# Optimization experiments

Measured on AMD Instinct MI355X. Metric: run time of the kernel, lower is better.

## Reference

```python
import jax, jax.numpy as jnp
import numpy as np

B = 256      # graph pairs
N = 256      # nodes per graph (uniform -> padding is a reshape)
DEG = 16     # avg degree
D = 32       # one_hot_dim
F1, F2, F3 = 128, 64, 64
T = 16       # tensor_neurons
BINS = 16
BOT = 16     # bottle_neck_neurons


def setup_inputs() -> dict:
    key = jax.random.key(0)
    ks = jax.random.split(key, 24)
    NT = B * N            # total nodes per side
    NE = B * N * DEG      # total directed edges per side
    x_q = jax.random.normal(ks[0], (NT, D), jnp.float32)
    x_c = jax.random.normal(ks[1], (NT, D), jnp.float32)
    edge_q = jax.random.randint(ks[2], (2, NE), 0, NT, jnp.int32)
    edge_c = jax.random.randint(ks[3], (2, NE), 0, NT, jnp.int32)
    qgraph_sizes = jnp.full((B,), N, jnp.int32)
    cgraph_sizes = jnp.full((B,), N, jnp.int32)

    def glorot(k, shape):
        fan = sum(shape[-2:]) if len(shape) >= 2 else shape[0] * 2
        return jax.random.uniform(k, shape, jnp.float32, -1.0, 1.0) * np.sqrt(6.0 / fan)

    params = dict(
        W1=glorot(ks[4], (D, F1)), b1=jnp.zeros((F1,), jnp.float32),
        W2=glorot(ks[5], (F1, F2)), b2=jnp.zeros((F2,), jnp.float32),
        W3=glorot(ks[6], (F2, F3)), b3=jnp.zeros((F3,), jnp.float32),
        attn_w=glorot(ks[7], (F3, F3)),
        ntn_a_w=glorot(ks[8], (T, F3, F3)),
        ntn_b_w=glorot(ks[9], (2 * F3, T)),
        ntn_bias=glorot(ks[10], (T, 1)),
        fc1_w=glorot(ks[11], (T + BINS, BOT)), fc1_b=jnp.zeros((BOT,), jnp.float32),
        fc2_w=glorot(ks[12], (BOT, 1)), fc2_b=jnp.zeros((1,), jnp.float32),
    )
    return dict(x_q=x_q, edge_q=edge_q, x_c=x_c, edge_c=edge_c,
                qgraph_sizes=qgraph_sizes, cgraph_sizes=cgraph_sizes, **params)


def _gcn(x, src, dst, W, b):
    n = x.shape[0]
    h = x @ W
    loop = jnp.arange(n, dtype=src.dtype)
    s = jnp.concatenate([src, loop])
    d = jnp.concatenate([dst, loop])
    deg = jax.ops.segment_sum(jnp.ones(s.shape, h.dtype), d, num_segments=n)
    dinv = jnp.where(deg > 0, jax.lax.rsqrt(jnp.maximum(deg, 1.0)), 0.0)
    coef = (dinv[s] * dinv[d])[:, None]
    return jax.ops.segment_sum(h[s] * coef, d, num_segments=n) + b


def _gnn(x, ei, W1, b1, W2, b2, W3, b3):
    src, dst = ei[0], ei[1]
    h = jax.nn.relu(_gcn(x, src, dst, W1, b1))        # dropout is identity in eval
    h = jax.nn.relu(_gcn(h, src, dst, W2, b2))
    return _gcn(h, src, dst, W3, b3)                  # [B*N, F3]


def _att_pool(q, attn_w, sizes):
    # q: [B, N, F3]
    ctx = jnp.tanh((q.sum(axis=1) @ attn_w) / sizes.astype(q.dtype)[:, None])  # [B, F3]
    sig = jax.nn.sigmoid(jnp.einsum('bnf,bf->bn', q, ctx))                      # [B, N]
    return jnp.einsum('bnf,bn->bf', q, sig)                                     # [B, F3]


def _pair_hist(q, c):
    # per-pair histogram of q @ c^T with BINS bins over each pair's [min, max]
    s = jax.lax.stop_gradient(jnp.einsum('bnf,bmf->bnm', q, c))  # [B, N, N]
    mn = s.min(axis=(1, 2), keepdims=True)
    mx = s.max(axis=(1, 2), keepdims=True)
    idx = jnp.clip(jnp.floor((s - mn) / jnp.maximum(mx - mn, 1e-12) * BINS),
                   0, BINS - 1).astype(jnp.int32)
    gid = (idx + jnp.arange(B, dtype=jnp.int32)[:, None, None] * BINS).reshape(-1)
    h = jax.ops.segment_sum(jnp.ones(gid.shape, jnp.float32), gid,
                            num_segments=B * BINS).reshape(B, BINS)
    return h / h.sum(axis=1, keepdims=True)


def reference(x_q, edge_q, x_c, edge_c, qgraph_sizes, cgraph_sizes,
              W1, b1, W2, b2, W3, b3, attn_w, ntn_a_w, ntn_b_w, ntn_bias,
              fc1_w, fc1_b, fc2_w, fc2_b):
    q = _gnn(x_q, edge_q, W1, b1, W2, b2, W3, b3).reshape(B, N, F3)
    c = _gnn(x_c, edge_c, W1, b1, W2, b2, W3, b3).reshape(B, N, F3)
    e1 = _att_pool(q, attn_w, qgraph_sizes)
    e2 = _att_pool(c, attn_w, cgraph_sizes)
    ntn = (jnp.einsum('bi,tij,bj->bt', e1, ntn_a_w, e2)
           + jnp.concatenate([e1, e2], axis=-1) @ ntn_b_w
           + ntn_bias[:, 0])
    scores = jax.nn.relu(ntn)                                   # [B, T]
    hist = _pair_hist(q, c)                                     # [B, BINS]
    scores = jnp.concatenate([scores, hist], axis=1)
    scores = jax.nn.relu(scores @ fc1_w + fc1_b)
    p = jax.nn.sigmoid(scores @ fc2_w + fc2_b)[:, 0]            # [B]
    ged = -0.5 * (qgraph_sizes + cgraph_sizes).astype(p.dtype) * jnp.log(p)
    return ged
```

## Files before the change

kernel.cpp:

```cpp
#include <hip/hip_runtime.h>
#include <hip/hip_bf16.h>
#include <math.h>

#define BB 256
#define NN 256
#define NT (BB*NN)
#define NT2 (2*NT)
#define NE (NT*16)
#define DD 32
#define F1C 128
#define F2C 64
#define F3C 64
#define TT 16
#define BINS 16

#define NBUCK 256
#define BSHIFT 9
#define BNODES 512
#define BCAP 10240
#define EPB 4096

typedef __attribute__((ext_vector_type(8))) short short8;
typedef __attribute__((ext_vector_type(4))) float f32x4;
typedef __attribute__((ext_vector_type(2))) float f32x2;

__device__ inline float b2f(ushort u) { return __uint_as_float(((uint)u) << 16); }
__device__ inline ushort f2b(float f) {
    uint u = __float_as_uint(f);
    return (ushort)((u + 0x7fffu + ((u >> 16) & 1u)) >> 16);
}
__device__ inline float clamp8(float v) { return fminf(fmaxf(v, -448.0f), 448.0f); }
__device__ inline uchar f2f8(float v) {
    int r = __builtin_amdgcn_cvt_pk_fp8_f32(clamp8(v), 0.0f, 0, false);
    return (uchar)(r & 0xff);
}
__device__ inline void f8x8_acc(uint2 w, float* acc) {
    f32x2 p;
    p = __builtin_amdgcn_cvt_pk_f32_fp8(w.x, false); acc[0] += p.x; acc[1] += p.y;
    p = __builtin_amdgcn_cvt_pk_f32_fp8(w.x, true);  acc[2] += p.x; acc[3] += p.y;
    p = __builtin_amdgcn_cvt_pk_f32_fp8(w.y, false); acc[4] += p.x; acc[5] += p.y;
    p = __builtin_amdgcn_cvt_pk_f32_fp8(w.y, true);  acc[6] += p.x; acc[7] += p.y;
}
__device__ inline uint2 f8x8_pack(const float* v) {
    uint2 r;
    r.x = (uint)__builtin_amdgcn_cvt_pk_fp8_f32(clamp8(v[0]), clamp8(v[1]), 0, false);
    r.x = (uint)__builtin_amdgcn_cvt_pk_fp8_f32(clamp8(v[2]), clamp8(v[3]), (int)r.x, true);
    r.y = (uint)__builtin_amdgcn_cvt_pk_fp8_f32(clamp8(v[4]), clamp8(v[5]), 0, false);
    r.y = (uint)__builtin_amdgcn_cvt_pk_fp8_f32(clamp8(v[6]), clamp8(v[7]), (int)r.y, true);
    return r;
}

__global__ __launch_bounds__(256) void prep_k(const float* __restrict__ W1, const float* __restrict__ W2,
                                              const float* __restrict__ W3, ushort* __restrict__ Wt1,
                                              ushort* __restrict__ Wt2, uchar* __restrict__ Wt3f8,
                                              int* __restrict__ gcount) {
    int i = blockIdx.x * 256 + threadIdx.x;
    if (i < NBUCK) gcount[i] = 0;
    if (i < DD * F1C)  { int k = i / F1C, n = i % F1C; Wt1[n * DD + k]  = f2b(W1[i]); }
    if (i < F1C * F2C) { int k = i / F2C, n = i % F2C; Wt2[n * F1C + k] = f2b(W2[i]); }
    if (i < F2C * F3C) { int k = i / F3C, n = i % F3C; Wt3f8[n * F2C + k] = f2f8(W3[i]); }
}

__global__ __launch_bounds__(256) void csr_p1_k(const int* __restrict__ eq, const int* __restrict__ ec,
                                                uint* __restrict__ staged, int* __restrict__ gcount) {
    __shared__ uint s_pk[EPB];
    __shared__ int s_cnt[NBUCK];
    __shared__ int s_off[NBUCK];
    __shared__ int s_base[NBUCK];
    __shared__ int s_gb[NBUCK];
    int t = threadIdx.x;
    bool sideB = blockIdx.x >= 256;
    const int* edge = sideB ? ec : eq;
    int off = sideB ? NT : 0;
    int e0 = (blockIdx.x & 255) * EPB;
    s_cnt[t] = 0;
    __syncthreads();
    uint pk[16]; int bk[16];
#pragma unroll
    for (int j = 0; j < 16; j++) {
        int e = e0 + j * 256 + t;
        int s = edge[e] + off;
        int d = edge[NE + e] + off;
        bk[j] = d >> BSHIFT;
        pk[j] = ((uint)s << BSHIFT) | (uint)(d & (BNODES - 1));
        atomicAdd(&s_cnt[bk[j]], 1);
    }
    __syncthreads();
    s_off[t] = s_cnt[t];
    __syncthreads();
    for (int o = 1; o < NBUCK; o <<= 1) {
        int x = (t >= o) ? s_off[t - o] : 0;
        __syncthreads();
        s_off[t] += x;
        __syncthreads();
    }
    {
        int ex = s_off[t] - s_cnt[t];
        s_base[t] = ex;
        s_off[t] = ex;
        s_gb[t] = atomicAdd(&gcount[t], s_cnt[t]);
    }
    __syncthreads();
#pragma unroll
    for (int j = 0; j < 16; j++) {
        int pos = atomicAdd(&s_off[bk[j]], 1);
        s_pk[pos] = pk[j];
    }
    __syncthreads();
    int w = t >> 6, l = t & 63;
    int bsel = l >> 4, l16 = l & 15;
    for (int pb = w; pb < NBUCK / 4; pb += 4) {
        int b = pb * 4 + bsel;
        int n = s_cnt[b], st = s_base[b], gb = s_gb[b];
        if (gb + n > BCAP) n = max(0, BCAP - gb);
        for (int i = l16; i < n; i += 16)
            staged[b * BCAP + gb + i] = s_pk[st + i];
    }
}

__global__ __launch_bounds__(256) void csr_p2_k(const uint* __restrict__ staged, const int* __restrict__ gcount,
                                                int* __restrict__ rp, int* __restrict__ indeg,
                                                float* __restrict__ dinv, int* __restrict__ ep) {
    int b = blockIdx.x;
    int t = threadIdx.x;
    __shared__ int cnt[BNODES];
    __shared__ int fl[BNODES];
    __shared__ int wsum[256];
    __shared__ int gsc[NBUCK];
    cnt[t] = 0; cnt[t + 256] = 0;
    gsc[t] = min(gcount[t], BCAP);
    __syncthreads();
    for (int off = 1; off < NBUCK; off <<= 1) {
        int x = (t >= off) ? gsc[t - off] : 0;
        __syncthreads();
        gsc[t] += x;
        __syncthreads();
    }
    int gbase = (b == 0) ? 0 : gsc[b - 1];
    int n = min(gcount[b], BCAP);
    const uint* sb = staged + (size_t)b * BCAP;
    int i = t;
    for (; i + 768 < n; i += 1024) {
        uint p0 = sb[i];
        uint p1 = sb[i + 256];
        uint p2 = sb[i + 512];
        uint p3 = sb[i + 768];
        atomicAdd(&cnt[p0 & (BNODES - 1)], 1);
        atomicAdd(&cnt[p1 & (BNODES - 1)], 1);
        atomicAdd(&cnt[p2 & (BNODES - 1)], 1);
        atomicAdd(&cnt[p3 & (BNODES - 1)], 1);
    }
    for (; i < n; i += 256)
        atomicAdd(&cnt[sb[i] & (BNODES - 1)], 1);
    __syncthreads();
    int base2 = t * 2;
    int c0 = cnt[base2], c1 = cnt[base2 + 1];
    int s2 = c0 + c1;
    wsum[t] = s2;
    __syncthreads();
    for (int off = 1; off < 256; off <<= 1) {
        int x = (t >= off) ? wsum[t - off] : 0;
        __syncthreads();
        wsum[t] += x;
        __syncthreads();
    }
    int p = gbase + wsum[t] - s2;
    int v0 = b * BNODES + base2;
    rp[v0] = p;          fl[base2] = p;
    indeg[v0] = c0;      dinv[v0] = rsqrtf((float)(c0 + 1));
    p += c0;
    rp[v0 + 1] = p;      fl[base2 + 1] = p;
    indeg[v0 + 1] = c1;  dinv[v0 + 1] = rsqrtf((float)(c1 + 1));
    __syncthreads();
    i = t;
    for (; i + 768 < n; i += 1024) {
        uint p0 = sb[i];
        uint p1 = sb[i + 256];
        uint p2 = sb[i + 512];
        uint p3 = sb[i + 768];
        ep[atomicAdd(&fl[p0 & (BNODES - 1)], 1)] = (int)(p0 >> BSHIFT);
        ep[atomicAdd(&fl[p1 & (BNODES - 1)], 1)] = (int)(p1 >> BSHIFT);
        ep[atomicAdd(&fl[p2 & (BNODES - 1)], 1)] = (int)(p2 >> BSHIFT);
        ep[atomicAdd(&fl[p3 & (BNODES - 1)], 1)] = (int)(p3 >> BSHIFT);
    }
    for (; i < n; i += 256) {
        uint pk = sb[i];
        ep[atomicAdd(&fl[pk & (BNODES - 1)], 1)] = (int)(pk >> BSHIFT);
    }
}

__global__ __launch_bounds__(256) void cvt2_k(const float* __restrict__ a, const float* __restrict__ b,
                                              const float* __restrict__ dinv, ushort* __restrict__ out) {
    int i = blockIdx.x * 256 + threadIdx.x;
    const int per = NT * DD / 4;
    bool sideB = i >= per;
    const float4* src = (const float4*)(sideB ? b : a);
    float4 v = src[sideB ? i - per : i];
    float dv = dinv[i / (DD / 4)];
    ushort4 o;
    o.x = f2b(v.x * dv); o.y = f2b(v.y * dv); o.z = f2b(v.z * dv); o.w = f2b(v.w * dv);
    ((ushort4*)out)[i] = o;
}

template<int F, bool BIAS, bool RELU>
__global__ __launch_bounds__(256) void agg_bf_k(const ushort* __restrict__ in, const int* __restrict__ rp,
                                                const int* __restrict__ indeg, const int* __restrict__ ep,
                                                const float* __restrict__ dinv,
                                                const float* __restrict__ bias, ushort* __restrict__ out) {
    constexpr int LPV = F / 8;
    constexpr int VPB = 256 / LPV;
    int g = threadIdx.x / LPV;
    int l = threadIdx.x % LPV;
    int v = blockIdx.x * VPB + g;
    float dv = dinv[v];
    short8 rs = *(const short8*)(in + (size_t)v * F + l * 8);
    float acc[8];
#pragma unroll
    for (int j = 0; j < 8; j++) acc[j] = b2f((ushort)rs[j]);
    int start = rp[v];
    int cnt   = indeg[v];
    int i = 0;
    for (; i + 4 <= cnt; i += 4) {
        int s0 = ep[start + i];
        int s1 = ep[start + i + 1];
        int s2 = ep[start + i + 2];
        int s3 = ep[start + i + 3];
        short8 r0 = *(const short8*)(in + (size_t)s0 * F + l * 8);
        short8 r1 = *(const short8*)(in + (size_t)s1 * F + l * 8);
        short8 r2 = *(const short8*)(in + (size_t)s2 * F + l * 8);
        short8 r3 = *(const short8*)(in + (size_t)s3 * F + l * 8);
#pragma unroll
        for (int j = 0; j < 8; j++) {
            acc[j] += b2f((ushort)r0[j]);
            acc[j] += b2f((ushort)r1[j]);
            acc[j] += b2f((ushort)r2[j]);
            acc[j] += b2f((ushort)r3[j]);
        }
    }
    for (; i < cnt; i++) {
        int s0 = ep[start + i];
        short8 r0 = *(const short8*)(in + (size_t)s0 * F + l * 8);
#pragma unroll
        for (int j = 0; j < 8; j++) acc[j] += b2f((ushort)r0[j]);
    }
    short8 o;
#pragma unroll
    for (int j = 0; j < 8; j++) {
        float x = dv * acc[j];
        if (BIAS) x += bias[l * 8 + j];
        if (RELU) x = fmaxf(x, 0.0f);
        o[j] = (short)f2b(x);
    }
    *(short8*)(out + (size_t)v * F + l * 8) = o;
}

template<bool OUT_BF16, bool BIAS, bool RELU>
__global__ __launch_bounds__(256) void agg_f8_k(const uchar* __restrict__ in, const int* __restrict__ rp,
                                                const int* __restrict__ indeg, const int* __restrict__ ep,
                                                const float* __restrict__ dinv,
                                                const float* __restrict__ bias, void* __restrict__ outp) {
    int g = threadIdx.x >> 3;
    int l = threadIdx.x & 7;
    int v = blockIdx.x * 32 + g;
    float dv = dinv[v];
    float acc[8] = {0, 0, 0, 0, 0, 0, 0, 0};
    f8x8_acc(*(const uint2*)(in + (size_t)v * 64 + l * 8), acc);
    int start = rp[v];
    int cnt   = indeg[v];
    int i = 0;
    for (; i + 4 <= cnt; i += 4) {
        int s0 = ep[start + i];
        int s1 = ep[start + i + 1];
        int s2 = ep[start + i + 2];
        int s3 = ep[start + i + 3];
        uint2 g0 = *(const uint2*)(in + (size_t)s0 * 64 + l * 8);
        uint2 g1 = *(const uint2*)(in + (size_t)s1 * 64 + l * 8);
        uint2 g2 = *(const uint2*)(in + (size_t)s2 * 64 + l * 8);
        uint2 g3 = *(const uint2*)(in + (size_t)s3 * 64 + l * 8);
        f8x8_acc(g0, acc); f8x8_acc(g1, acc); f8x8_acc(g2, acc); f8x8_acc(g3, acc);
    }
    for (; i < cnt; i++) {
        int s0 = ep[start + i];
        f8x8_acc(*(const uint2*)(in + (size_t)s0 * 64 + l * 8), acc);
    }
#pragma unroll
    for (int j = 0; j < 8; j++) {
        float x = dv * acc[j];
        if (BIAS) x += bias[l * 8 + j];
        if (RELU) x = fmaxf(x, 0.0f);
        acc[j] = x;
    }
    if (OUT_BF16) {
        short8 o;
#pragma unroll
        for (int j = 0; j < 8; j++) o[j] = (short)f2b(acc[j]);
        *(short8*)((ushort*)outp + (size_t)v * 64 + l * 8) = o;
    } else {
        *(uint2*)((uchar*)outp + (size_t)v * 64 + l * 8) = f8x8_pack(acc);
    }
}

template<int K, int N, bool BIAS, bool RELU, bool SCALE, bool OUT8>
__global__ __launch_bounds__(256) void gemm_mfma_k(const ushort* __restrict__ A,
                                                   const ushort* __restrict__ Wt,
                                                   const float* __restrict__ bias,
                                                   const float* __restrict__ dinv,
                                                   void* __restrict__ outp) {
    constexpr int KC = K / 32;
    int w = threadIdx.x >> 6, lane = threadIdx.x & 63;
    int r16 = lane & 15, koff = (lane >> 4) * 8;
    size_t rows0 = (size_t)blockIdx.x * 128;

    short8 af[KC][2];
#pragma unroll
    for (int kc = 0; kc < KC; kc++)
#pragma unroll
        for (int mt = 0; mt < 2; mt++)
            af[kc][mt] = *(const short8*)(A + (rows0 + (w * 2 + mt) * 16 + r16) * K + kc * 32 + koff);

    float dvr[2][4];
#pragma unroll
    for (int mt = 0; mt < 2; mt++)
#pragma unroll
        for (int r = 0; r < 4; r++)
            dvr[mt][r] = SCALE ? dinv[rows0 + (w * 2 + mt) * 16 + (lane >> 4) * 4 + r] : 1.0f;

#pragma unroll
    for (int nt = 0; nt < N / 16; nt++) {
        f32x4 acc[2] = {{0.f,0.f,0.f,0.f},{0.f,0.f,0.f,0.f}};
#pragma unroll
        for (int kc = 0; kc < KC; kc++) {
            short8 b = *(const short8*)(Wt + (size_t)(nt * 16 + r16) * K + kc * 32 + koff);
            acc[0] = __builtin_amdgcn_mfma_f32_16x16x32_bf16(af[kc][0], b, acc[0], 0, 0, 0);
            acc[1] = __builtin_amdgcn_mfma_f32_16x16x32_bf16(af[kc][1], b, acc[1], 0, 0, 0);
        }
#pragma unroll
        for (int mt = 0; mt < 2; mt++) {
#pragma unroll
            for (int r = 0; r < 4; r++) {
                size_t row = rows0 + (w * 2 + mt) * 16 + (lane >> 4) * 4 + r;
                int col = nt * 16 + (lane & 15);
                float v = acc[mt][r];
                if (BIAS) v += bias[col];
                if (RELU) v = fmaxf(v, 0.0f);
                if (SCALE) v *= dvr[mt][r];
                if (OUT8) ((uchar*)outp)[row * N + col] = f2f8(v);
                else      ((ushort*)outp)[row * N + col] = f2b(v);
            }
        }
    }
}

__global__ __launch_bounds__(256) void gemm_f8_k(const uchar* __restrict__ A8,
                                                 const uchar* __restrict__ Wt8,
                                                 const float* __restrict__ dinv,
                                                 uchar* __restrict__ out8) {
    int w = threadIdx.x >> 6, lane = threadIdx.x & 63;
    int r16 = lane & 15, koff = (lane >> 4) * 8;
    size_t rows0 = (size_t)blockIdx.x * 128;

    long af[2][2];
#pragma unroll
    for (int kc = 0; kc < 2; kc++)
#pragma unroll
        for (int mt = 0; mt < 2; mt++)
            af[kc][mt] = *(const long*)(A8 + (rows0 + (w * 2 + mt) * 16 + r16) * 64 + kc * 32 + koff);

    float dvr[2][4];
#pragma unroll
    for (int mt = 0; mt < 2; mt++)
#pragma unroll
        for (int r = 0; r < 4; r++)
            dvr[mt][r] = dinv[rows0 + (w * 2 + mt) * 16 + (lane >> 4) * 4 + r];

#pragma unroll
    for (int nt = 0; nt < 4; nt++) {
        f32x4 acc[2] = {{0.f,0.f,0.f,0.f},{0.f,0.f,0.f,0.f}};
#pragma unroll
        for (int kc = 0; kc < 2; kc++) {
            long b = *(const long*)(Wt8 + (size_t)(nt * 16 + r16) * 64 + kc * 32 + koff);
            acc[0] = __builtin_amdgcn_mfma_f32_16x16x32_fp8_fp8(af[kc][0], b, acc[0], 0, 0, 0);
            acc[1] = __builtin_amdgcn_mfma_f32_16x16x32_fp8_fp8(af[kc][1], b, acc[1], 0, 0, 0);
        }
#pragma unroll
        for (int mt = 0; mt < 2; mt++) {
#pragma unroll
            for (int r = 0; r < 4; r++) {
                size_t row = rows0 + (w * 2 + mt) * 16 + (lane >> 4) * 4 + r;
                int col = nt * 16 + (lane & 15);
                out8[row * 64 + col] = f2f8(acc[mt][r] * dvr[mt][r]);
            }
        }
    }
}

__global__ __launch_bounds__(256) void pool_k(const ushort* __restrict__ fin,
                                              const int* __restrict__ qsz, const int* __restrict__ csz,
                                              const float* __restrict__ attn_w, float* __restrict__ e_out) {
    int b = blockIdx.x & 255;
    bool is_c = blockIdx.x >= BB;
    const ushort* emb = fin + (size_t)blockIdx.x * NN * F3C;
    float size = (float)((is_c ? csz : qsz)[b]);
    float* eo = e_out + (is_c ? BB * F3C : 0) + b * F3C;

    int t = threadIdx.x;
    int f = t & 63;
    int w = t >> 6;

    __shared__ float s_emb[NN][F3C + 1];
    __shared__ float s_red[4][64];
    __shared__ float s_sq[64];
    __shared__ float s_ctx[64];
    __shared__ float s_sig[NN];

    float psum = 0.0f;
    for (int n = w; n < NN; n += 4) {
        float v = b2f(emb[n * F3C + f]);
        s_emb[n][f] = v;
        psum += v;
    }
    s_red[w][f] = psum;
    __syncthreads();

    if (w == 0) {
        s_sq[f] = s_red[0][f] + s_red[1][f] + s_red[2][f] + s_red[3][f];
        float acc = 0.0f;
        for (int k = 0; k < 64; k++) acc += s_sq[k] * attn_w[k * 64 + f];
        s_ctx[f] = tanhf(acc / size);
    }
    __syncthreads();

    {
        float acc = 0.0f;
#pragma unroll 8
        for (int k = 0; k < 64; k++) acc += s_emb[t][k] * s_ctx[k];
        s_sig[t] = 1.0f / (1.0f + expf(-acc));
    }
    __syncthreads();

    float eacc = 0.0f;
#pragma unroll 8
    for (int i = 0; i < 64; i++) {
        int n = w * 64 + i;
        eacc += s_sig[n] * s_emb[n][f];
    }
    s_red[w][f] = eacc;
    __syncthreads();
    if (w == 0) eo[f] = s_red[0][f] + s_red[1][f] + s_red[2][f] + s_red[3][f];
}

__global__ __launch_bounds__(256) void hist_k(const ushort* __restrict__ qbf, const ushort* __restrict__ cbf,
                                              float* __restrict__ histp) {
    int b = blockIdx.x;
    const ushort* qb = qbf + (size_t)b * NN * 64;
    const ushort* cb = cbf + (size_t)b * NN * 64;
    int lane = threadIdx.x & 63;
    int w = threadIdx.x >> 6;
    int r16 = lane & 15, koff = (lane >> 4) * 8;

    short8 a[4][2];
#pragma unroll
    for (int i = 0; i < 4; i++) {
        int row = (w * 4 + i) * 16 + r16;
#pragma unroll
        for (int kk = 0; kk < 2; kk++)
            a[i][kk] = *(const short8*)(qb + row * 64 + kk * 32 + koff);
    }

    float mn = 1e30f, mx = -1e30f;
    for (int mt = 0; mt < 16; mt++) {
        int crow = mt * 16 + r16;
        short8 b0 = *(const short8*)(cb + crow * 64 + koff);
        short8 b1 = *(const short8*)(cb + crow * 64 + 32 + koff);
#pragma unroll
        for (int i = 0; i < 4; i++) {
            f32x4 acc = {0.0f, 0.0f, 0.0f, 0.0f};
            acc = __builtin_amdgcn_mfma_f32_16x16x32_bf16(a[i][0], b0, acc, 0, 0, 0);
            acc = __builtin_amdgcn_mfma_f32_16x16x32_bf16(a[i][1], b1, acc, 0, 0, 0);
            mn = fminf(mn, fminf(fminf(acc[0], acc[1]), fminf(acc[2], acc[3])));
            mx = fmaxf(mx, fmaxf(fmaxf(acc[0], acc[1]), fmaxf(acc[2], acc[3])));
        }
    }
    for (int off = 32; off; off >>= 1) {
        mn = fminf(mn, __shfl_xor(mn, off, 64));
        mx = fmaxf(mx, __shfl_xor(mx, off, 64));
    }
    __shared__ float smn[4], smx[4];
    __shared__ float s_mn, s_scale;
    if (lane == 0) { smn[w] = mn; smx[w] = mx; }
    __syncthreads();
    if (threadIdx.x == 0) {
        float m0 = fminf(fminf(smn[0], smn[1]), fminf(smn[2], smn[3]));
        float m1 = fmaxf(fmaxf(smx[0], smx[1]), fmaxf(smx[2], smx[3]));
        s_mn = m0;
        s_scale = 16.0f / fmaxf(m1 - m0, 1e-12f);
    }
    __shared__ int h[16 * 256];
#pragma unroll
    for (int i = 0; i < 16; i++) h[i * 256 + threadIdx.x] = 0;
    __syncthreads();
    float bmn = s_mn, bscale = s_scale;

    for (int mt = 0; mt < 16; mt++) {
        int crow = mt * 16 + r16;
        short8 b0 = *(const short8*)(cb + crow * 64 + koff);
        short8 b1 = *(const short8*)(cb + crow * 64 + 32 + koff);
#pragma unroll
        for (int i = 0; i < 4; i++) {
            f32x4 acc = {0.0f, 0.0f, 0.0f, 0.0f};
            acc = __builtin_amdgcn_mfma_f32_16x16x32_bf16(a[i][0], b0, acc, 0, 0, 0);
            acc = __builtin_amdgcn_mfma_f32_16x16x32_bf16(a[i][1], b1, acc, 0, 0, 0);
#pragma unroll
            for (int r = 0; r < 4; r++) {
                int bin = (int)floorf((acc[r] - bmn) * bscale);
                bin = min(max(bin, 0), 15);
                h[bin * 256 + threadIdx.x] += 1;
            }
        }
    }
    __syncthreads();
    __shared__ int hp[16][16];
    int bb = threadIdx.x >> 4, part = threadIdx.x & 15;
    int sum = 0;
#pragma unroll
    for (int j = 0; j < 16; j++) sum += h[bb * 256 + part * 16 + j];
    hp[bb][part] = sum;
    __syncthreads();
    if (threadIdx.x < 16) {
        int s = 0;
#pragma unroll
        for (int j = 0; j < 16; j++) s += hp[threadIdx.x][j];
        histp[b * 16 + threadIdx.x] = (float)s;
    }
}

__global__ __launch_bounds__(256) void ntn_final_k(const float* __restrict__ e, const float* __restrict__ A,
                                                   const float* __restrict__ bw, const float* __restrict__ bias,
                                                   const float* __restrict__ histp,
                                                   const float* __restrict__ fc1w, const float* __restrict__ fc1b,
                                                   const float* __restrict__ fc2w, const float* __restrict__ fc2b,
                                                   const int* __restrict__ qsz, const int* __restrict__ csz,
                                                   float* __restrict__ out) {
    int b = blockIdx.x;
    int t = threadIdx.x;
    __shared__ float s_e1[64], s_e2[64];
    __shared__ float s_ntn[16];
    __shared__ float s_s[32];
    __shared__ float s_a[16];
    if (t < 64) s_e1[t] = e[b * 64 + t];
    else if (t < 128) s_e2[t - 64] = e[BB * 64 + b * 64 + (t - 64)];
    if (t < 16) s_ntn[t] = 0.0f;
    __syncthreads();
#pragma unroll
    for (int r = 0; r < 4; r++) {
        int idx = t + r * 256;
        int tt = idx >> 6, i = idx & 63;
        const float* Ar = A + (size_t)idx * 64;
        float acc = 0.0f;
        for (int j = 0; j < 64; j++) acc += Ar[j] * s_e2[j];
        atomicAdd(&s_ntn[tt], s_e1[i] * acc);
    }
    __syncthreads();
    if (t < 16) {
        float acc = s_ntn[t] + bias[t];
        for (int k = 0; k < 64; k++) acc += s_e1[k] * bw[k * 16 + t];
        for (int k = 0; k < 64; k++) acc += s_e2[k] * bw[(64 + k) * 16 + t];
        s_s[t] = fmaxf(acc, 0.0f);
        s_s[16 + t] = histp[b * 16 + t] * (1.0f / 65536.0f);
    }
    __syncthreads();
    if (t < 16) {
        float a = fc1b[t];
        for (int k = 0; k < 32; k++) a += s_s[k] * fc1w[k * 16 + t];
        s_a[t] = fmaxf(a, 0.0f);
    }
    __syncthreads();
    if (t == 0) {
        float z = fc2b[0];
        for (int j = 0; j < 16; j++) z += s_a[j] * fc2w[j];
        float nz = -z;
        float sp = (nz > 20.0f) ? nz : log1pf(expf(nz));
        out[b] = 0.5f * (float)(qsz[b] + csz[b]) * sp;
    }
}

extern "C" void kernel_launch(void* const* d_in, const int* in_sizes, int n_in,
                              void* d_out, int out_size, void* d_ws, size_t ws_size,
                              hipStream_t stream) {
    const float* x_q    = (const float*)d_in[0];
    const int*   edge_q = (const int*)d_in[1];
    const float* x_c    = (const float*)d_in[2];
    const int*   edge_c = (const int*)d_in[3];
    const int*   qsz    = (const int*)d_in[4];
    const int*   csz    = (const int*)d_in[5];
    const float* W1 = (const float*)d_in[6];
    const float* b1 = (const float*)d_in[7];
    const float* W2 = (const float*)d_in[8];
    const float* b2 = (const float*)d_in[9];
    const float* W3 = (const float*)d_in[10];
    const float* b3 = (const float*)d_in[11];
    const float* attn_w  = (const float*)d_in[12];
    const float* ntn_a   = (const float*)d_in[13];
    const float* ntn_b   = (const float*)d_in[14];
    const float* ntn_bias= (const float*)d_in[15];
    const float* fc1w = (const float*)d_in[16];
    const float* fc1b = (const float*)d_in[17];
    const float* fc2w = (const float*)d_in[18];
    const float* fc2b = (const float*)d_in[19];
    float* out = (float*)d_out;

    char* w = (char*)d_ws;
    auto alloc = [&](size_t bytes) -> void* {
        void* p = (void*)w;
        w += (bytes + 255) & ~(size_t)255;
        return p;
    };
    int*    rp     = (int*)alloc((size_t)NT2 * 4);
    int*    indeg  = (int*)alloc((size_t)NT2 * 4);
    float*  dinv   = (float*)alloc((size_t)NT2 * 4);
    int*    gcount = (int*)alloc(NBUCK * 4);
    uint*   staged = (uint*)alloc((size_t)NBUCK * BCAP * 4);
    int*    ep     = (int*)alloc((size_t)2 * NE * 4);
    ushort* xb     = (ushort*)alloc((size_t)NT2 * 32 * 2);
    ushort* xa     = (ushort*)alloc((size_t)NT2 * 32 * 2);
    ushort* hA     = (ushort*)alloc((size_t)NT2 * 128 * 2);
    uchar*  h8a    = (uchar*)alloc((size_t)NT2 * 64);
    uchar*  h8b    = (uchar*)alloc((size_t)NT2 * 64);
    ushort* fin    = (ushort*)alloc((size_t)NT2 * 64 * 2);
    ushort* Wt1    = (ushort*)alloc((size_t)DD * F1C * 2);
    ushort* Wt2    = (ushort*)alloc((size_t)F1C * F2C * 2);
    uchar*  Wt3f8  = (uchar*)alloc((size_t)F2C * F3C);
    float*  e12    = (float*)alloc(2 * BB * 64 * 4);
    float*  histp  = (float*)alloc(256 * 16 * 4);
    ushort* qfin = fin;
    ushort* cfin = fin + (size_t)NT * 64;

    prep_k<<<32, 256, 0, stream>>>(W1, W2, W3, Wt1, Wt2, Wt3f8, gcount);
    csr_p1_k<<<512, 256, 0, stream>>>(edge_q, edge_c, staged, gcount);
    csr_p2_k<<<NBUCK, 256, 0, stream>>>(staged, gcount, rp, indeg, dinv, ep);

    cvt2_k<<<NT2 * 32 / 4 / 256, 256, 0, stream>>>(x_q, x_c, dinv, xb);

    agg_bf_k<32, false, false><<<NT2 / 64, 256, 0, stream>>>(xb, rp, indeg, ep, dinv, nullptr, xa);
    gemm_mfma_k<32, 128, true, true, false, false><<<NT2 / 128, 256, 0, stream>>>(xa, Wt1, b1, nullptr, hA);
    gemm_mfma_k<128, 64, false, false, true, true><<<NT2 / 128, 256, 0, stream>>>(hA, Wt2, nullptr, dinv, h8a);
    agg_f8_k<false, true, true><<<NT2 / 32, 256, 0, stream>>>(h8a, rp, indeg, ep, dinv, b2, h8b);
    gemm_f8_k<<<NT2 / 128, 256, 0, stream>>>(h8b, Wt3f8, dinv, h8a);
    agg_f8_k<true, true, false><<<NT2 / 32, 256, 0, stream>>>(h8a, rp, indeg, ep, dinv, b3, fin);

    pool_k<<<2 * BB, 256, 0, stream>>>(fin, qsz, csz, attn_w, e12);
    hist_k<<<BB, 256, 0, stream>>>(qfin, cfin, histp);
    ntn_final_k<<<BB, 256, 0, stream>>>(e12, ntn_a, ntn_b, ntn_bias, histp,
                                        fc1w, fc1b, fc2w, fc2b, qsz, csz, out);
}
```

Measured before the change: 319.4 us.

## Fuse layer-1/2 GEMMs through LDS and merge small kernels

```diff
diff --git a/kernel.cpp b/kernel.cpp
--- a/kernel.cpp
+++ b/kernel.cpp
@@ -50,15 +50,8 @@
     return r;
 }
 
-__global__ __launch_bounds__(256) void prep_k(const float* __restrict__ W1, const float* __restrict__ W2,
-                                              const float* __restrict__ W3, ushort* __restrict__ Wt1,
-                                              ushort* __restrict__ Wt2, uchar* __restrict__ Wt3f8,
-                                              int* __restrict__ gcount) {
-    int i = blockIdx.x * 256 + threadIdx.x;
-    if (i < NBUCK) gcount[i] = 0;
-    if (i < DD * F1C)  { int k = i / F1C, n = i % F1C; Wt1[n * DD + k]  = f2b(W1[i]); }
-    if (i < F1C * F2C) { int k = i / F2C, n = i % F2C; Wt2[n * F1C + k] = f2b(W2[i]); }
-    if (i < F2C * F3C) { int k = i / F3C, n = i % F3C; Wt3f8[n * F2C + k] = f2f8(W3[i]); }
+__global__ __launch_bounds__(256) void zero_k(int* __restrict__ gcount) {
+    gcount[threadIdx.x] = 0;
 }
 
 __global__ __launch_bounds__(256) void csr_p1_k(const int* __restrict__ eq, const int* __restrict__ ec,
@@ -189,17 +182,28 @@
     }
 }
 
-__global__ __launch_bounds__(256) void cvt2_k(const float* __restrict__ a, const float* __restrict__ b,
-                                              const float* __restrict__ dinv, ushort* __restrict__ out) {
-    int i = blockIdx.x * 256 + threadIdx.x;
-    const int per = NT * DD / 4;
-    bool sideB = i >= per;
-    const float4* src = (const float4*)(sideB ? b : a);
-    float4 v = src[sideB ? i - per : i];
-    float dv = dinv[i / (DD / 4)];
-    ushort4 o;
-    o.x = f2b(v.x * dv); o.y = f2b(v.y * dv); o.z = f2b(v.z * dv); o.w = f2b(v.w * dv);
-    ((ushort4*)out)[i] = o;
+__global__ __launch_bounds__(256) void cvt2w_k(const float* __restrict__ a, const float* __restrict__ b,
+                                               const float* __restrict__ dinv, ushort* __restrict__ out,
+                                               const float* __restrict__ W1, const float* __restrict__ W2,
+                                               const float* __restrict__ W3, ushort* __restrict__ Wt1,
+                                               ushort* __restrict__ Wt2, uchar* __restrict__ Wt3f8) {
+    const int NB_X = NT2 * DD / 4 / 256;
+    if (blockIdx.x < NB_X) {
+        int i = blockIdx.x * 256 + threadIdx.x;
+        const int per = NT * DD / 4;
+        bool sideB = i >= per;
+        const float4* src = (const float4*)(sideB ? b : a);
+        float4 v = src[sideB ? i - per : i];
+        float dv = dinv[i / (DD / 4)];
+        ushort4 o;
+        o.x = f2b(v.x * dv); o.y = f2b(v.y * dv); o.z = f2b(v.z * dv); o.w = f2b(v.w * dv);
+        ((ushort4*)out)[i] = o;
+    } else {
+        int i = (blockIdx.x - NB_X) * 256 + threadIdx.x;
+        if (i < DD * F1C)  { int k = i / F1C, n = i % F1C; Wt1[n * DD + k]  = f2b(W1[i]); }
+        if (i < F1C * F2C) { int k = i / F2C, n = i % F2C; Wt2[n * F1C + k] = f2b(W2[i]); }
+        if (i < F2C * F3C) { int k = i / F3C, n = i % F3C; Wt3f8[n * F2C + k] = f2f8(W3[i]); }
+    }
 }
 
 template<int F, bool BIAS, bool RELU>
@@ -300,54 +304,68 @@
     }
 }
 
-template<int K, int N, bool BIAS, bool RELU, bool SCALE, bool OUT8>
-__global__ __launch_bounds__(256) void gemm_mfma_k(const ushort* __restrict__ A,
-                                                   const ushort* __restrict__ Wt,
-                                                   const float* __restrict__ bias,
-                                                   const float* __restrict__ dinv,
-                                                   void* __restrict__ outp) {
-    constexpr int KC = K / 32;
+__global__ __launch_bounds__(256) void gemm12_k(const ushort* __restrict__ xa,
+                                                const ushort* __restrict__ Wt1,
+                                                const float* __restrict__ b1,
+                                                const ushort* __restrict__ Wt2,
+                                                const float* __restrict__ dinv,
+                                                uchar* __restrict__ h8a) {
+    __shared__ ushort s_h1[128][136];
     int w = threadIdx.x >> 6, lane = threadIdx.x & 63;
-    int r16 = lane & 15, koff = (lane >> 4) * 8;
+    int r16 = lane & 15, quad = lane >> 4, koff = quad * 8;
     size_t rows0 = (size_t)blockIdx.x * 128;
 
-    short8 af[KC][2];
-#pragma unroll
-    for (int kc = 0; kc < KC; kc++)
+    short8 af1[2];
+#pragma unroll
+    for (int mt = 0; mt < 2; mt++)
+        af1[mt] = *(const short8*)(xa + (rows0 + (w * 2 + mt) * 16 + r16) * 32 + koff);
+#pragma unroll
+    for (int nt = 0; nt < 8; nt++) {
+        short8 bfr = *(const short8*)(Wt1 + (size_t)(nt * 16 + r16) * 32 + koff);
+        f32x4 acc[2] = {{0.f,0.f,0.f,0.f},{0.f,0.f,0.f,0.f}};
+        acc[0] = __builtin_amdgcn_mfma_f32_16x16x32_bf16(af1[0], bfr, acc[0], 0, 0, 0);
+        acc[1] = __builtin_amdgcn_mfma_f32_16x16x32_bf16(af1[1], bfr, acc[1], 0, 0, 0);
+        int col = nt * 16 + r16;
+        float bc = b1[col];
 #pragma unroll
         for (int mt = 0; mt < 2; mt++)
-            af[kc][mt] = *(const short8*)(A + (rows0 + (w * 2 + mt) * 16 + r16) * K + kc * 32 + koff);
-
+#pragma unroll
+            for (int r = 0; r < 4; r++) {
+                int rl = (w * 2 + mt) * 16 + quad * 4 + r;
+                s_h1[rl][col] = f2b(fmaxf(acc[mt][r] + bc, 0.0f));
+            }
+    }
+    __syncthreads();
+
+    short8 af2[4][2];
+#pragma unroll
+    for (int kc = 0; kc < 4; kc++)
+#pragma unroll
+        for (int mt = 0; mt < 2; mt++)
+            af2[kc][mt] = *(const short8*)&s_h1[(w * 2 + mt) * 16 + r16][kc * 32 + koff];
     float dvr[2][4];
 #pragma unroll
     for (int mt = 0; mt < 2; mt++)
 #pragma unroll
         for (int r = 0; r < 4; r++)
-            dvr[mt][r] = SCALE ? dinv[rows0 + (w * 2 + mt) * 16 + (lane >> 4) * 4 + r] : 1.0f;
-
-#pragma unroll
-    for (int nt = 0; nt < N / 16; nt++) {
+            dvr[mt][r] = dinv[rows0 + (w * 2 + mt) * 16 + quad * 4 + r];
+#pragma unroll
+    for (int nt = 0; nt < 4; nt++) {
         f32x4 acc[2] = {{0.f,0.f,0.f,0.f},{0.f,0.f,0.f,0.f}};
 #pragma unroll
-        for (int kc = 0; kc < KC; kc++) {
-            short8 b = *(const short8*)(Wt + (size_t)(nt * 16 + r16) * K + kc * 32 + koff);
-            acc[0] = __builtin_amdgcn_mfma_f32_16x16x32_bf16(af[kc][0], b, acc[0], 0, 0, 0);
-            acc[1] = __builtin_amdgcn_mfma_f32_16x16x32_bf16(af[kc][1], b, acc[1], 0, 0, 0);
-        }
-#pragma unroll
-        for (int mt = 0; mt < 2; mt++) {
+        for (int kc = 0; kc < 4; kc++) {
+            short8 bfr = *(const short8*)(Wt2 + (size_t)(nt * 16 + r16) * 128 + kc * 32 + koff);
+            acc[0] = __builtin_amdgcn_mfma_f32_16x16x32_bf16(af2[kc][0], bfr, acc[0], 0, 0, 0);
+            acc[1] = __builtin_amdgcn_mfma_f32_16x16x32_bf16(af2[kc][1], bfr, acc[1], 0, 0, 0);
+        }
+#pragma unroll
+        for (int mt = 0; mt < 2; mt++)
 #pragma unroll
             for (int r = 0; r < 4; r++) {
-                size_t row = rows0 + (w * 2 + mt) * 16 + (lane >> 4) * 4 + r;
-                int col = nt * 16 + (lane & 15);
-                float v = acc[mt][r];
-                if (BIAS) v += bias[col];
-                if (RELU) v = fmaxf(v, 0.0f);
-                if (SCALE) v *= dvr[mt][r];
-                if (OUT8) ((uchar*)outp)[row * N + col] = f2f8(v);
-                else      ((ushort*)outp)[row * N + col] = f2b(v);
+                size_t row = rows0 + (w * 2 + mt) * 16 + quad * 4 + r;
+                int col = nt * 16 + r16;
+                h8a[row * 64 + col] = f2f8(acc[mt][r] * dvr[mt][r]);
             }
-        }
     }
 }
 
@@ -394,143 +412,137 @@
     }
 }
 
-__global__ __launch_bounds__(256) void pool_k(const ushort* __restrict__ fin,
-                                              const int* __restrict__ qsz, const int* __restrict__ csz,
-                                              const float* __restrict__ attn_w, float* __restrict__ e_out) {
-    int b = blockIdx.x & 255;
-    bool is_c = blockIdx.x >= BB;
-    const ushort* emb = fin + (size_t)blockIdx.x * NN * F3C;
-    float size = (float)((is_c ? csz : qsz)[b]);
-    float* eo = e_out + (is_c ? BB * F3C : 0) + b * F3C;
-
+__global__ __launch_bounds__(256) void pool_hist_k(const ushort* __restrict__ fin,
+                                                   const int* __restrict__ qsz, const int* __restrict__ csz,
+                                                   const float* __restrict__ attn_w,
+                                                   float* __restrict__ e_out, float* __restrict__ histp) {
+    __shared__ float smemf[17472];
     int t = threadIdx.x;
-    int f = t & 63;
-    int w = t >> 6;
-
-    __shared__ float s_emb[NN][F3C + 1];
-    __shared__ float s_red[4][64];
-    __shared__ float s_sq[64];
-    __shared__ float s_ctx[64];
-    __shared__ float s_sig[NN];
-
-    float psum = 0.0f;
-    for (int n = w; n < NN; n += 4) {
-        float v = b2f(emb[n * F3C + f]);
-        s_emb[n][f] = v;
-        psum += v;
-    }
-    s_red[w][f] = psum;
-    __syncthreads();
-
-    if (w == 0) {
-        s_sq[f] = s_red[0][f] + s_red[1][f] + s_red[2][f] + s_red[3][f];
-        float acc = 0.0f;
-        for (int k = 0; k < 64; k++) acc += s_sq[k] * attn_w[k * 64 + f];
-        s_ctx[f] = tanhf(acc / size);
-    }
-    __syncthreads();
-
-    {
-        float acc = 0.0f;
+    if (blockIdx.x < 512) {
+        int b = blockIdx.x & 255;
+        bool is_c = blockIdx.x >= BB;
+        const ushort* emb = fin + (size_t)blockIdx.x * NN * F3C;
+        float size = (float)((is_c ? csz : qsz)[b]);
+        float* eo = e_out + (is_c ? BB * F3C : 0) + b * F3C;
+        float (*s_emb)[F3C + 1] = (float(*)[F3C + 1])smemf;
+        float* s_red = smemf + 256 * 65;
+        float* s_sq  = s_red + 256;
+        float* s_ctx = s_sq + 64;
+        float* s_sig = s_ctx + 64;
+        int f = t & 63;
+        int w = t >> 6;
+        float psum = 0.0f;
+        for (int n = w; n < NN; n += 4) {
+            float v = b2f(emb[n * F3C + f]);
+            s_emb[n][f] = v;
+            psum += v;
+        }
+        s_red[w * 64 + f] = psum;
+        __syncthreads();
+        if (w == 0) {
+            s_sq[f] = s_red[f] + s_red[64 + f] + s_red[128 + f] + s_red[192 + f];
+            float acc = 0.0f;
+            for (int k = 0; k < 64; k++) acc += s_sq[k] * attn_w[k * 64 + f];
+            s_ctx[f] = tanhf(acc / size);
+        }
+        __syncthreads();
+        {
+            float acc = 0.0f;
 #pragma unroll 8
-        for (int k = 0; k < 64; k++) acc += s_emb[t][k] * s_ctx[k];
-        s_sig[t] = 1.0f / (1.0f + expf(-acc));
-    }
-    __syncthreads();
-
-    float eacc = 0.0f;
+            for (int k = 0; k < 64; k++) acc += s_emb[t][k] * s_ctx[k];
+            s_sig[t] = 1.0f / (1.0f + expf(-acc));
+        }
+        __syncthreads();
+        float eacc = 0.0f;
 #pragma unroll 8
-    for (int i = 0; i < 64; i++) {
-        int n = w * 64 + i;
-        eacc += s_sig[n] * s_emb[n][f];
-    }
-    s_red[w][f] = eacc;
-    __syncthreads();
-    if (w == 0) eo[f] = s_red[0][f] + s_red[1][f] + s_red[2][f] + s_red[3][f];
-}
-
-__global__ __launch_bounds__(256) void hist_k(const ushort* __restrict__ qbf, const ushort* __restrict__ cbf,
-                                              float* __restrict__ histp) {
-    int b = blockIdx.x;
-    const ushort* qb = qbf + (size_t)b * NN * 64;
-    const ushort* cb = cbf + (size_t)b * NN * 64;
-    int lane = threadIdx.x & 63;
-    int w = threadIdx.x >> 6;
-    int r16 = lane & 15, koff = (lane >> 4) * 8;
-
-    short8 a[4][2];
-#pragma unroll
-    for (int i = 0; i < 4; i++) {
-        int row = (w * 4 + i) * 16 + r16;
-#pragma unroll
-        for (int kk = 0; kk < 2; kk++)
-            a[i][kk] = *(const short8*)(qb + row * 64 + kk * 32 + koff);
-    }
-
-    float mn = 1e30f, mx = -1e30f;
-    for (int mt = 0; mt < 16; mt++) {
-        int crow = mt * 16 + r16;
-        short8 b0 = *(const short8*)(cb + crow * 64 + koff);
-        short8 b1 = *(const short8*)(cb + crow * 64 + 32 + koff);
+        for (int i = 0; i < 64; i++) {
+            int n = w * 64 + i;
+            eacc += s_sig[n] * s_emb[n][f];
+        }
+        s_red[w * 64 + f] = eacc;
+        __syncthreads();
+        if (w == 0) eo[f] = s_red[f] + s_red[64 + f] + s_red[128 + f] + s_red[192 + f];
+    } else {
+        int b = blockIdx.x - 512;
+        const ushort* qb = fin + (size_t)b * NN * 64;
+        const ushort* cb = fin + (size_t)(NT + b * NN) * 64;
+        int lane = t & 63;
+        int w = t >> 6;
+        int r16 = lane & 15, koff = (lane >> 4) * 8;
+        int* h = (int*)smemf;
+        int* hp = h + 16 * 256;
+        float* smn = (float*)(hp + 256);
+        float* smx = smn + 4;
+        float* s_sc = smx + 4;
+
+        short8 a[4][2];
 #pragma unroll
         for (int i = 0; i < 4; i++) {
-            f32x4 acc = {0.0f, 0.0f, 0.0f, 0.0f};
-            acc = __builtin_amdgcn_mfma_f32_16x16x32_bf16(a[i][0], b0, acc, 0, 0, 0);
-            acc = __builtin_amdgcn_mfma_f32_16x16x32_bf16(a[i][1], b1, acc, 0, 0, 0);
-            mn = fminf(mn, fminf(fminf(acc[0], acc[1]), fminf(acc[2], acc[3])));
-            mx = fmaxf(mx, fmaxf(fmaxf(acc[0], acc[1]), fmaxf(acc[2], acc[3])));
-        }
-    }
-    for (int off = 32; off; off >>= 1) {
-        mn = fminf(mn, __shfl_xor(mn, off, 64));
-        mx = fmaxf(mx, __shfl_xor(mx, off, 64));
-    }
-    __shared__ float smn[4], smx[4];
-    __shared__ float s_mn, s_scale;
-    if (lane == 0) { smn[w] = mn; smx[w] = mx; }
-    __syncthreads();
-    if (threadIdx.x == 0) {
-        float m0 = fminf(fminf(smn[0], smn[1]), fminf(smn[2], smn[3]));
-        float m1 = fmaxf(fmaxf(smx[0], smx[1]), fmaxf(smx[2], smx[3]));
-        s_mn = m0;
-        s_scale = 16.0f / fmaxf(m1 - m0, 1e-12f);
-    }
-    __shared__ int h[16 * 256];
-#pragma unroll
-    for (int i = 0; i < 16; i++) h[i * 256 + threadIdx.x] = 0;
-    __syncthreads();
-    float bmn = s_mn, bscale = s_scale;
-
-    for (int mt = 0; mt < 16; mt++) {
-        int crow = mt * 16 + r16;
-        short8 b0 = *(const short8*)(cb + crow * 64 + koff);
-        short8 b1 = *(const short8*)(cb + crow * 64 + 32 + koff);
-#pragma unroll
-        for (int i = 0; i < 4; i++) {
-            f32x4 acc = {0.0f, 0.0f, 0.0f, 0.0f};
-            acc = __builtin_amdgcn_mfma_f32_16x16x32_bf16(a[i][0], b0, acc, 0, 0, 0);
-            acc = __builtin_amdgcn_mfma_f32_16x16x32_bf16(a[i][1], b1, acc, 0, 0, 0);
-#pragma unroll
-            for (int r = 0; r < 4; r++) {
-                int bin = (int)floorf((acc[r] - bmn) * bscale);
-                bin = min(max(bin, 0), 15);
-                h[bin * 256 + threadIdx.x] += 1;
+            int row = (w * 4 + i) * 16 + r16;
+#pragma unroll
+            for (int kk = 0; kk < 2; kk++)
+                a[i][kk] = *(const short8*)(qb + row * 64 + kk * 32 + koff);
+        }
+        float mn = 1e30f, mx = -1e30f;
+        for (int mt = 0; mt < 16; mt++) {
+            int crow = mt * 16 + r16;
+            short8 b0 = *(const short8*)(cb + crow * 64 + koff);
+            short8 b1 = *(const short8*)(cb + crow * 64 + 32 + koff);
+#pragma unroll
+            for (int i = 0; i < 4; i++) {
+                f32x4 acc = {0.0f, 0.0f, 0.0f, 0.0f};
+                acc = __builtin_amdgcn_mfma_f32_16x16x32_bf16(a[i][0], b0, acc, 0, 0, 0);
+                acc = __builtin_amdgcn_mfma_f32_16x16x32_bf16(a[i][1], b1, acc, 0, 0, 0);
+                mn = fminf(mn, fminf(fminf(acc[0], acc[1]), fminf(acc[2], acc[3])));
+                mx = fmaxf(mx, fmaxf(fmaxf(acc[0], acc[1]), fmaxf(acc[2], acc[3])));
             }
         }
-    }
-    __syncthreads();
-    __shared__ int hp[16][16];
-    int bb = threadIdx.x >> 4, part = threadIdx.x & 15;
-    int sum = 0;
-#pragma unroll
-    for (int j = 0; j < 16; j++) sum += h[bb * 256 + part * 16 + j];
-    hp[bb][part] = sum;
-    __syncthreads();
-    if (threadIdx.x < 16) {
-        int s = 0;
-#pragma unroll
-        for (int j = 0; j < 16; j++) s += hp[threadIdx.x][j];
-        histp[b * 16 + threadIdx.x] = (float)s;
+        for (int off = 32; off; off >>= 1) {
+            mn = fminf(mn, __shfl_xor(mn, off, 64));
+            mx = fmaxf(mx, __shfl_xor(mx, off, 64));
+        }
+        if (lane == 0) { smn[w] = mn; smx[w] = mx; }
+        __syncthreads();
+        if (t == 0) {
+            float m0 = fminf(fminf(smn[0], smn[1]), fminf(smn[2], smn[3]));
+            float m1 = fmaxf(fmaxf(smx[0], smx[1]), fmaxf(smx[2], smx[3]));
+            s_sc[0] = m0;
+            s_sc[1] = 16.0f / fmaxf(m1 - m0, 1e-12f);
+        }
+#pragma unroll
+        for (int i = 0; i < 16; i++) h[i * 256 + t] = 0;
+        __syncthreads();
+        float bmn = s_sc[0], bscale = s_sc[1];
+        for (int mt = 0; mt < 16; mt++) {
+            int crow = mt * 16 + r16;
+            short8 b0 = *(const short8*)(cb + crow * 64 + koff);
+            short8 b1 = *(const short8*)(cb + crow * 64 + 32 + koff);
+#pragma unroll
+            for (int i = 0; i < 4; i++) {
+                f32x4 acc = {0.0f, 0.0f, 0.0f, 0.0f};
+                acc = __builtin_amdgcn_mfma_f32_16x16x32_bf16(a[i][0], b0, acc, 0, 0, 0);
+                acc = __builtin_amdgcn_mfma_f32_16x16x32_bf16(a[i][1], b1, acc, 0, 0, 0);
+#pragma unroll
+                for (int r = 0; r < 4; r++) {
+                    int bin = (int)floorf((acc[r] - bmn) * bscale);
+                    bin = min(max(bin, 0), 15);
+                    h[bin * 256 + t] += 1;
+                }
+            }
+        }
+        __syncthreads();
+        int bb = t >> 4, part = t & 15;
+        int sum = 0;
+#pragma unroll
+        for (int j = 0; j < 16; j++) sum += h[bb * 256 + part * 16 + j];
+        hp[bb * 16 + part] = sum;
+        __syncthreads();
+        if (t < 16) {
+            int s = 0;
+#pragma unroll
+            for (int j = 0; j < 16; j++) s += hp[t * 16 + j];
+            histp[b * 16 + t] = (float)s;
+        }
     }
 }
 
@@ -623,7 +635,6 @@
     int*    ep     = (int*)alloc((size_t)2 * NE * 4);
     ushort* xb     = (ushort*)alloc((size_t)NT2 * 32 * 2);
     ushort* xa     = (ushort*)alloc((size_t)NT2 * 32 * 2);
-    ushort* hA     = (ushort*)alloc((size_t)NT2 * 128 * 2);
     uchar*  h8a    = (uchar*)alloc((size_t)NT2 * 64);
     uchar*  h8b    = (uchar*)alloc((size_t)NT2 * 64);
     ushort* fin    = (ushort*)alloc((size_t)NT2 * 64 * 2);
@@ -632,24 +643,21 @@
     uchar*  Wt3f8  = (uchar*)alloc((size_t)F2C * F3C);
     float*  e12    = (float*)alloc(2 * BB * 64 * 4);
     float*  histp  = (float*)alloc(256 * 16 * 4);
-    ushort* qfin = fin;
-    ushort* cfin = fin + (size_t)NT * 64;
-
-    prep_k<<<32, 256, 0, stream>>>(W1, W2, W3, Wt1, Wt2, Wt3f8, gcount);
+
+    zero_k<<<1, 256, 0, stream>>>(gcount);
     csr_p1_k<<<512, 256, 0, stream>>>(edge_q, edge_c, staged, gcount);
     csr_p2_k<<<NBUCK, 256, 0, stream>>>(staged, gcount, rp, indeg, dinv, ep);
 
-    cvt2_k<<<NT2 * 32 / 4 / 256, 256, 0, stream>>>(x_q, x_c, dinv, xb);
+    cvt2w_k<<<NT2 * 32 / 4 / 256 + 64, 256, 0, stream>>>(x_q, x_c, dinv, xb,
+                                                         W1, W2, W3, Wt1, Wt2, Wt3f8);
 
     agg_bf_k<32, false, false><<<NT2 / 64, 256, 0, stream>>>(xb, rp, indeg, ep, dinv, nullptr, xa);
-    gemm_mfma_k<32, 128, true, true, false, false><<<NT2 / 128, 256, 0, stream>>>(xa, Wt1, b1, nullptr, hA);
-    gemm_mfma_k<128, 64, false, false, true, true><<<NT2 / 128, 256, 0, stream>>>(hA, Wt2, nullptr, dinv, h8a);
+    gemm12_k<<<NT2 / 128, 256, 0, stream>>>(xa, Wt1, b1, Wt2, dinv, h8a);
     agg_f8_k<false, true, true><<<NT2 / 32, 256, 0, stream>>>(h8a, rp, indeg, ep, dinv, b2, h8b);
     gemm_f8_k<<<NT2 / 128, 256, 0, stream>>>(h8b, Wt3f8, dinv, h8a);
     agg_f8_k<true, true, false><<<NT2 / 32, 256, 0, stream>>>(h8a, rp, indeg, ep, dinv, b3, fin);
 
-    pool_k<<<2 * BB, 256, 0, stream>>>(fin, qsz, csz, attn_w, e12);
-    hist_k<<<BB, 256, 0, stream>>>(qfin, cfin, histp);
+    pool_hist_k<<<768, 256, 0, stream>>>(fin, qsz, csz, attn_w, e12, histp);
     ntn_final_k<<<BB, 256, 0, stream>>>(e12, ntn_a, ntn_b, ntn_bias, histp,
                                         fc1w, fc1b, fc2w, fc2b, qsz, csz, out);
 }
```

Result: faster. 306.5 us (-4.0%).
